# Kernel tuning notes

Hardware: AMD Instinct MI355X
Metric: run time of the kernel (lower is better)

The kernel has to match this reference:

```python
import jax, jax.numpy as jnp
import numpy as np

D_MODEL = 256
D_EDGE = 64
EPS = 1e-05
INPUT_FEATS = 2 * D_MODEL + D_EDGE + 1  # 577


def _linear_params(key, fan_in, fan_out):
    k1, k2 = jax.random.split(key)
    lim = 1.0 / np.sqrt(fan_in)
    W = jax.random.uniform(k1, (fan_in, fan_out), minval=-lim, maxval=lim, dtype=jnp.float32)
    b = jax.random.uniform(k2, (fan_out,), minval=-lim, maxval=lim, dtype=jnp.float32)
    return W, b


def setup_inputs() -> dict:
    key = jax.random.key(0)
    ks = jax.random.split(key, 16)
    B, N = 8, 128
    inp = {
        "coords": jax.random.normal(ks[0], (B, N, 3), dtype=jnp.float32),
        "inv_feats": jax.random.normal(ks[1], (B, N, D_MODEL), dtype=jnp.float32),
        "adj_matrix": jnp.ones((B, N, N), dtype=jnp.float32),
        "atom_mask": jnp.ones((B, N), dtype=jnp.float32),
        "edge_feats": jax.random.normal(ks[2], (B, N, N, D_EDGE), dtype=jnp.float32),
    }
    inp["W_e1"], inp["b_e1"] = _linear_params(ks[3], INPUT_FEATS, D_MODEL)
    inp["W_e2"], inp["b_e2"] = _linear_params(ks[4], D_MODEL, D_MODEL)
    inp["W_att"], inp["b_att"] = _linear_params(ks[5], D_MODEL, 1)
    inp["W_h1"], inp["b_h1"] = _linear_params(ks[6], 2 * D_MODEL, D_MODEL)
    inp["W_h2"], inp["b_h2"] = _linear_params(ks[7], D_MODEL, D_MODEL)
    inp["W_x1"], inp["b_x1"] = _linear_params(ks[8], INPUT_FEATS, D_MODEL)
    inp["W_x2"], inp["b_x2"] = _linear_params(ks[9], D_MODEL, D_MODEL)
    inp["W_x3"], inp["b_x3"] = _linear_params(ks[10], D_MODEL, 1)
    return inp


def _pair_linear(W, b, node_feats, ef):
    # Linear over concat([node_i, node_j, ef]) without materializing the concat.
    # W: [2*d_model + d_edge + 1, out]
    d = D_MODEL
    hi = node_feats @ W[:d]          # [B,N,out]
    hj = node_feats @ W[d:2 * d]     # [B,N,out]
    he = ef @ W[2 * d:]              # [B,N,N,out]
    return hi[:, :, None, :] + hj[:, None, :, :] + he + b


def _egnn_forward(coords, inv_feats, adj_matrix, atom_mask, edge_feats,
                  W_e1, b_e1, W_e2, b_e2, W_att, b_att,
                  W_h1, b_h1, W_h2, b_h2, W_x1, b_x1, W_x2, b_x2, W_x3, b_x3):
    mask = atom_mask[..., None]                       # [B,N,1]
    diff = coords[:, :, None, :] - coords[:, None, :, :]   # [B,N,N,3]
    sq = jnp.sum(diff * diff, axis=-1, keepdims=True)      # [B,N,N,1]
    ef = jnp.concatenate([edge_feats, sq], axis=-1)        # [B,N,N,d_edge+1]
    adj = adj_matrix[..., None]                             # [B,N,N,1]

    # phi_e: Linear-SiLU-Linear-SiLU on pair features
    msg = jax.nn.silu(_pair_linear(W_e1, b_e1, inv_feats, ef))
    msg = jax.nn.silu(msg @ W_e2 + b_e2)                    # [B,N,N,d]

    att = jax.nn.sigmoid(msg @ W_att + b_att)               # [B,N,N,1]
    node_msg = jnp.sum(msg * att * adj, axis=2)             # [B,N,d]

    h = jnp.concatenate([inv_feats, node_msg], axis=-1)
    h = jax.nn.silu(h @ W_h1 + b_h1) @ W_h2 + b_h2          # [B,N,d]

    # phi_x: Linear-SiLU-Linear-SiLU-Linear -> scalar per edge
    ex = jax.nn.silu(_pair_linear(W_x1, b_x1, inv_feats, ef))
    ex = jax.nn.silu(ex @ W_x2 + b_x2)
    edge_attn = ex @ W_x3 + b_x3                             # [B,N,N,1]

    normalisers = jnp.sqrt(sq[..., 0] + EPS) + 1.0           # [B,N,N]
    weighted = diff * edge_attn / normalisers[..., None] * adj
    coord_updates = jnp.sum(weighted, axis=2)                # [B,N,3]
    num_nodes = jnp.sum(mask, axis=1) + 1.0                  # [B,1]
    coord_updates = coord_updates / num_nodes[:, :, None]

    out_coords = (coords + coord_updates) * mask
    out_feats = h * mask
    return out_coords, out_feats


def reference(coords, inv_feats, adj_matrix, atom_mask, edge_feats,
              W_e1, b_e1, W_e2, b_e2, W_att, b_att,
              W_h1, b_h1, W_h2, b_h2, W_x1, b_x1, W_x2, b_x2, W_x3, b_x3):
    return _egnn_forward(coords, inv_feats, adj_matrix, atom_mask, edge_feats,
                         W_e1, b_e1, W_e2, b_e2, W_att, b_att,
                         W_h1, b_h1, W_h2, b_h2, W_x1, b_x1, W_x2, b_x2, W_x3, b_x3)
```

## Files before the change

kernel.cpp:

```cpp
#include <hip/hip_runtime.h>

typedef __attribute__((ext_vector_type(8))) __bf16 bf16x8;
typedef __attribute__((ext_vector_type(4))) __bf16 bf16x4;
typedef __attribute__((ext_vector_type(4))) float f32x4;

#define SCHED0 __builtin_amdgcn_sched_barrier(0)

__device__ __forceinline__ float fast_sig(float x) {
  return __builtin_amdgcn_rcpf(1.0f + __expf(-x));
}
__device__ __forceinline__ float siluf(float x) { return x * fast_sig(x); }
__device__ __forceinline__ __bf16 tobf(float x) { return (__bf16)x; }

__device__ __forceinline__ void stage16(const void* g, void* l) {
  __builtin_amdgcn_global_load_lds(
      (const __attribute__((address_space(1))) void*)g,
      (__attribute__((address_space(3))) void*)l, 16, 0, 0);
}

__device__ __forceinline__ void stage_slice(
    const __bf16* __restrict__ src, int ld, int off,
    __bf16* swbuf, int tid)
{
  const int w = tid >> 6;
  #pragma unroll
  for (int q = 0; q < 2; q++) {
    int t16 = q * 512 + tid;
    int c = t16 >> 2, slot = t16 & 3;
    int kpart = slot ^ ((c >> 1) & 3);
    const __bf16* g = src + (size_t)c * ld + off + kpart * 8;
    __bf16* l = swbuf + (size_t)(q * 512 + w * 64) * 8;
    stage16(g, l);
  }
}

__device__ __forceinline__ void stage_k(
    const __bf16* __restrict__ wt, const __bf16* __restrict__ w2,
    int k, __bf16* buf, int tid)
{
  if (k < 2) stage_slice(wt, 576, 512 + k * 32, buf, tid);
  else       stage_slice(w2, 256, (k - 2) * 32, buf, tid);
}

__global__ __launch_bounds__(256) void k_prep(
    const float* __restrict__ We1, const float* __restrict__ Wx1,
    const float* __restrict__ We2, const float* __restrict__ Wx2,
    const float* __restrict__ Wh1, const float* __restrict__ Wh2,
    const float* __restrict__ invf,
    __bf16* __restrict__ wt_e, __bf16* __restrict__ wt_x,
    __bf16* __restrict__ w2e, __bf16* __restrict__ w2x,
    __bf16* __restrict__ wh1t, __bf16* __restrict__ wh2t,
    __bf16* __restrict__ invb,
    float* __restrict__ nmsg, float* __restrict__ cupd)
{
  int idx = blockIdx.x * 256 + threadIdx.x;
  if (idx < 147456) {
    int kk = idx / 576, f = idx - kk * 576;
    wt_e[idx] = tobf(We1[f * 256 + kk]);
    wt_x[idx] = tobf(Wx1[f * 256 + kk]);
  }
  if (idx < 65536) {
    int c = idx >> 8, k = idx & 255;
    w2e[idx] = tobf(We2[k * 256 + c]);
    w2x[idx] = tobf(Wx2[k * 256 + c]);
    wh2t[idx] = tobf(Wh2[k * 256 + c]);
    f32x4 z = {0.f, 0.f, 0.f, 0.f};
    *(f32x4*)(nmsg + idx * 4) = z;
  }
  if (idx < 131072) {
    int c = idx >> 9, k = idx & 511;
    wh1t[idx] = tobf(Wh1[k * 256 + c]);
  }
  if (idx < 3072) cupd[idx] = 0.f;
  invb[idx] = tobf(invf[idx]);
}

template<int NKS>
__device__ __forceinline__ void node_gemm64(
    const __bf16* __restrict__ B, int ldb, int boff,
    const __bf16* __restrict__ A, int lda, int aoff,
    int row0, int tid, f32x4 acc[4][4])
{
  const int lane = tid & 63, wc = tid >> 6, lr = lane & 15, lg = lane >> 4;
  #pragma unroll
  for (int ks = 0; ks < NKS; ks++) {
    bf16x8 bB[4], aA[4];
    #pragma unroll
    for (int m = 0; m < 4; m++)
      bB[m] = *(const bf16x8*)(B + (size_t)(row0 + m * 16 + lr) * ldb + boff + ks * 32 + lg * 8);
    #pragma unroll
    for (int n = 0; n < 4; n++)
      aA[n] = *(const bf16x8*)(A + (size_t)(wc * 64 + n * 16 + lr) * lda + aoff + ks * 32 + lg * 8);
    #pragma unroll
    for (int m = 0; m < 4; m++)
      #pragma unroll
      for (int n = 0; n < 4; n++)
        acc[m][n] = __builtin_amdgcn_mfma_f32_16x16x32_bf16(aA[n], bB[m], acc[m][n], 0, 0, 0);
  }
}

__global__ __launch_bounds__(256) void k_nproj(
    const __bf16* __restrict__ invb,
    const __bf16* __restrict__ wt_e, const __bf16* __restrict__ wt_x,
    const float* __restrict__ be1, const float* __restrict__ bx1,
    float* __restrict__ hie, float* __restrict__ hix,
    __bf16* __restrict__ hje, __bf16* __restrict__ hjx)
{
  const int tid = threadIdx.x;
  const int row0 = blockIdx.x * 64;
  const int mat = blockIdx.y;
  const __bf16* A = (mat < 2) ? wt_e : wt_x;
  const int aoff = (mat & 1) ? 256 : 0;

  f32x4 acc[4][4];
  #pragma unroll
  for (int m = 0; m < 4; m++)
    #pragma unroll
    for (int n = 0; n < 4; n++) { f32x4 z = {0.f,0.f,0.f,0.f}; acc[m][n] = z; }
  node_gemm64<8>(invb, 256, 0, A, 576, aoff, row0, tid, acc);

  const int lane = tid & 63, wc = tid >> 6, lr = lane & 15, lg = lane >> 4;
  if ((mat & 1) == 0) {
    const float* bias = (mat == 0) ? be1 : bx1;
    float* out = (mat == 0) ? hie : hix;
    #pragma unroll
    for (int m = 0; m < 4; m++) {
      int node = row0 + m * 16 + lr;
      #pragma unroll
      for (int n = 0; n < 4; n++) {
        int c0 = wc * 64 + n * 16 + lg * 4;
        f32x4 v = acc[m][n] + *(const f32x4*)(bias + c0);
        *(f32x4*)(out + (size_t)node * 256 + c0) = v;
      }
    }
  } else {
    __bf16* out = (mat == 1) ? hje : hjx;
    #pragma unroll
    for (int m = 0; m < 4; m++) {
      int node = row0 + m * 16 + lr;
      #pragma unroll
      for (int n = 0; n < 4; n++) {
        int c0 = wc * 64 + n * 16 + lg * 4;
        bf16x4 pk;
        #pragma unroll
        for (int r = 0; r < 4; r++) pk[r] = tobf(acc[m][n][r]);
        *(bf16x4*)(out + (size_t)node * 256 + c0) = pk;
      }
    }
  }
}

__global__ __launch_bounds__(256) void k_h1(
    const __bf16* __restrict__ invb, const float* __restrict__ nmsg,
    const __bf16* __restrict__ wh1t,
    const float* __restrict__ bh1, __bf16* __restrict__ h1b)
{
  const int tid = threadIdx.x;
  const int row0 = blockIdx.x * 64;
  const int c0 = blockIdx.y * 64;
  const int lane = tid & 63, w = tid >> 6, lr = lane & 15, lg = lane >> 4;
  const int node = row0 + w * 16 + lr;

  f32x4 acc[4];
  #pragma unroll
  for (int n = 0; n < 4; n++) { f32x4 z = {0.f,0.f,0.f,0.f}; acc[n] = z; }

  #pragma unroll
  for (int ks = 0; ks < 16; ks++) {
    bf16x8 bB;
    if (ks < 8) {
      bB = *(const bf16x8*)(invb + (size_t)node * 256 + ks * 32 + lg * 8);
    } else {
      const float* pp = nmsg + (size_t)node * 256 + (ks - 8) * 32 + lg * 8;
      f32x4 lo = *(const f32x4*)pp;
      f32x4 hi = *(const f32x4*)(pp + 4);
      bf16x8 t;
      t[0]=tobf(lo[0]); t[1]=tobf(lo[1]); t[2]=tobf(lo[2]); t[3]=tobf(lo[3]);
      t[4]=tobf(hi[0]); t[5]=tobf(hi[1]); t[6]=tobf(hi[2]); t[7]=tobf(hi[3]);
      bB = t;
    }
    #pragma unroll
    for (int n = 0; n < 4; n++) {
      bf16x8 aA = *(const bf16x8*)(wh1t + (size_t)(c0 + n * 16 + lr) * 512 + ks * 32 + lg * 8);
      acc[n] = __builtin_amdgcn_mfma_f32_16x16x32_bf16(aA, bB, acc[n], 0, 0, 0);
    }
  }

  #pragma unroll
  for (int n = 0; n < 4; n++) {
    int cc = c0 + n * 16 + lg * 4;
    f32x4 b4 = *(const f32x4*)(bh1 + cc);
    bf16x4 pk;
    #pragma unroll
    for (int r = 0; r < 4; r++) pk[r] = tobf(siluf(acc[n][r] + b4[r]));
    *(bf16x4*)(h1b + (size_t)node * 256 + cc) = pk;
  }
}

__global__ __launch_bounds__(256) void k_h2(
    const __bf16* __restrict__ h1b, const __bf16* __restrict__ wh2t,
    const float* __restrict__ bh2, const float* __restrict__ amask,
    const float* __restrict__ coords, const float* __restrict__ cupd,
    float* __restrict__ out_feats, float* __restrict__ out_coords)
{
  __shared__ float sM[2];
  const int tid = threadIdx.x;
  const int row0 = blockIdx.x * 64;
  const int c0 = blockIdx.y * 64;
  const int b = row0 >> 7;
  const int lane = tid & 63, w = tid >> 6, lr = lane & 15, lg = lane >> 4;
  const int node = row0 + w * 16 + lr;

  f32x4 acc[4];
  #pragma unroll
  for (int n = 0; n < 4; n++) { f32x4 z = {0.f,0.f,0.f,0.f}; acc[n] = z; }

  #pragma unroll
  for (int ks = 0; ks < 8; ks++) {
    bf16x8 bB = *(const bf16x8*)(h1b + (size_t)node * 256 + ks * 32 + lg * 8);
    #pragma unroll
    for (int n = 0; n < 4; n++) {
      bf16x8 aA = *(const bf16x8*)(wh2t + (size_t)(c0 + n * 16 + lr) * 256 + ks * 32 + lg * 8);
      acc[n] = __builtin_amdgcn_mfma_f32_16x16x32_bf16(aA, bB, acc[n], 0, 0, 0);
    }
  }

  float msk = amask[node];
  #pragma unroll
  for (int n = 0; n < 4; n++) {
    int cc = c0 + n * 16 + lg * 4;
    f32x4 b4 = *(const f32x4*)(bh2 + cc);
    f32x4 v = (acc[n] + b4) * msk;
    *(f32x4*)(out_feats + (size_t)node * 256 + cc) = v;
  }

  if (blockIdx.y == 0) {
    if (tid < 128) {
      float v = amask[b * 128 + tid];
      #pragma unroll
      for (int off = 1; off < 64; off <<= 1) v += __shfl_xor(v, off);
      if ((tid & 63) == 0) sM[tid >> 6] = v;
    }
    __syncthreads();
    const float sNum = sM[0] + sM[1];
    if (tid < 192) {
      int nl = tid / 3, d = tid - nl * 3;
      int nd = row0 + nl;
      float upd = cupd[nd * 3 + d] / (sNum + 1.0f);
      out_coords[nd * 3 + d] = (coords[nd * 3 + d] + upd) * amask[nd];
    }
  }
}

__global__ __launch_bounds__(512, 4) void k_edge(
    const float* __restrict__ coords, const float* __restrict__ adjm,
    const float* __restrict__ ef,
    const float* __restrict__ We1, const float* __restrict__ Wx1,
    const float* __restrict__ batt,
    const float* __restrict__ be2, const float* __restrict__ bx2,
    const float* __restrict__ bx3,
    const float* __restrict__ Watt, const float* __restrict__ Wx3,
    const float* __restrict__ hie, const float* __restrict__ hix,
    const __bf16* __restrict__ hje, const __bf16* __restrict__ hjx,
    const __bf16* __restrict__ wt_e, const __bf16* __restrict__ wt_x,
    const __bf16* __restrict__ w2e, const __bf16* __restrict__ w2x,
    float* __restrict__ nmsg, float* __restrict__ cupd)
{
  __shared__ __align__(16) char sSb[64 * 512];
  __shared__ __align__(16) __bf16 sW0[8192];
  __shared__ __align__(16) __bf16 sW1[8192];
  __shared__ __align__(16) __bf16 sE[64 * 72];
  __shared__ float slaste[256], slastx[256];
  __shared__ float sqv[64], sAdj[64], sRedE[64], sRedX[64], sNM[256], sCup[4];

  const int tid = threadIdx.x;
  const int raw = blockIdx.x;
  const int lb = (raw & 7) * 256 + (raw >> 3);
  const int bi = lb >> 1;
  const int half = lb & 1;
  const int b = bi >> 7;
  const int j0g = half * 64;
  const int jg0 = b * 128 + j0g;

  const int lane = tid & 63, w = tid >> 6;
  const int lr = lane & 15, lg = lane >> 4;
  const int cg = (w & 3) * 64;
  const int jw = (w >> 2) * 32;
  const int slot = lg ^ ((lr >> 1) & 3);
  const int awbase = (cg + lr) * 32 + slot * 8;

  const float cix = coords[bi * 3 + 0];
  const float ciy = coords[bi * 3 + 1];
  const float ciz = coords[bi * 3 + 2];
  const float b0e = batt[0];
  const float b0x = bx3[0];

  if (tid < 64) { sRedE[tid] = 0.f; sRedX[tid] = 0.f; }
  else if (tid < 320) sNM[tid - 64] = 0.f;
  else if (tid < 324) sCup[tid - 320] = 0.f;
  if (tid < 256) {
    slaste[tid] = We1[576 * 256 + tid];
    slastx[tid] = Wx1[576 * 256 + tid];
  }
  if (tid >= 448) {
    int j = tid - 448;
    int jg = jg0 + j;
    float dx = cix - coords[jg * 3 + 0];
    float dy = ciy - coords[jg * 3 + 1];
    float dz = ciz - coords[jg * 3 + 2];
    sqv[j] = dx * dx + dy * dy + dz * dz;
  }
  if (tid >= 384 && tid < 448)
    sAdj[tid - 384] = adjm[(size_t)bi * 128 + j0g + (tid - 384)];

  {
    const float* efb = ef + ((size_t)bi * 128 + j0g) * 64;
    int row = tid >> 3;
    int col = (tid & 7) * 8;
    const float* er = efb + row * 64 + col;
    f32x4 x = *(const f32x4*)er;
    f32x4 y = *(const f32x4*)(er + 4);
    bf16x8 t;
    t[0] = tobf(x[0]); t[1] = tobf(x[1]); t[2] = tobf(x[2]); t[3] = tobf(x[3]);
    t[4] = tobf(y[0]); t[5] = tobf(y[1]); t[6] = tobf(y[2]); t[7] = tobf(y[3]);
    *(bf16x8*)(sE + row * 72 + col) = t;
  }

  stage_k(wt_e, w2e, 0, sW0, tid);
  stage_k(wt_e, w2e, 1, sW1, tid);

  asm volatile("s_waitcnt lgkmcnt(0)" ::: "memory");
  SCHED0;

  #pragma unroll
  for (int p = 0; p < 2; p++) {
    const __bf16* wt = p ? wt_x : wt_e;
    const __bf16* w2 = p ? w2x : w2e;
    const float* hi_g = (p ? hix : hie) + (size_t)bi * 256;
    const __bf16* hj_g = (p ? hjx : hje) + (size_t)jg0 * 256;
    const float* slast = p ? slastx : slaste;
    const float* bias2 = p ? bx2 : be2;
    const float* vvec = p ? Wx3 : Watt;
    float* sRed = p ? sRedX : sRedE;
    const float batt0 = p ? b0x : b0e;

    f32x4 acc[2][4];
    #pragma unroll
    for (int m = 0; m < 2; m++)
      #pragma unroll
      for (int n = 0; n < 4; n++) { f32x4 z = {0.f,0.f,0.f,0.f}; acc[m][n] = z; }

    #pragma unroll
    for (int k = 0; k < 10; k++) {
      SCHED0;
      if (k < 9) asm volatile("s_waitcnt vmcnt(2)" ::: "memory");
      else       asm volatile("s_waitcnt vmcnt(0)" ::: "memory");
      SCHED0;
      __builtin_amdgcn_s_barrier();
      SCHED0;

      __bf16* sw = (k & 1) ? sW1 : sW0;
      bf16x8 aW[4];
      #pragma unroll
      for (int n = 0; n < 4; n++) aW[n] = *(const bf16x8*)(sw + awbase + n * 512);

      if (k < 2) {
        bf16x8 bEf[2];
        #pragma unroll
        for (int m = 0; m < 2; m++)
          bEf[m] = *(const bf16x8*)(sE + (jw + m * 16 + lr) * 72 + k * 32 + lg * 8);
        __builtin_amdgcn_s_setprio(1);
        #pragma unroll
        for (int m = 0; m < 2; m++)
          #pragma unroll
          for (int n = 0; n < 4; n++)
            acc[m][n] = __builtin_amdgcn_mfma_f32_16x16x32_bf16(aW[n], bEf[m], acc[m][n], 0, 0, 0);
        __builtin_amdgcn_s_setprio(0);
        if (k == 1) {
          f32x4 hi4[4];
          bf16x4 hj4[2][4];
          #pragma unroll
          for (int n = 0; n < 4; n++)
            hi4[n] = *(const f32x4*)(hi_g + cg + n * 16 + lg * 4);
          #pragma unroll
          for (int m = 0; m < 2; m++) {
            const int jl = jw + m * 16 + lr;
            #pragma unroll
            for (int n = 0; n < 4; n++)
              hj4[m][n] = *(const bf16x4*)(hj_g + (size_t)jl * 256 + cg + n * 16 + lg * 4);
          }
          #pragma unroll
          for (int m = 0; m < 2; m++) {
            const int jl = jw + m * 16 + lr;
            const float sq = sqv[jl];
            #pragma unroll
            for (int n = 0; n < 4; n++) {
              const int kk0 = cg + n * 16 + lg * 4;
              f32x4 sl4 = *(const f32x4*)(slast + kk0);
              bf16x4 pk;
              #pragma unroll
              for (int r = 0; r < 4; r++) {
                float v = acc[m][n][r] + hi4[n][r] + (float)hj4[m][n][r] + sq * sl4[r];
                pk[r] = tobf(siluf(v));
              }
              int off = (jl * 512 + kk0 * 2) ^ ((jl & 7) << 4);
              *(bf16x4*)(sSb + off) = pk;
              f32x4 z = {0.f, 0.f, 0.f, 0.f};
              acc[m][n] = z;
            }
          }
        }
      } else {
        const int ks = k - 2;
        bf16x8 bS[2];
        #pragma unroll
        for (int m = 0; m < 2; m++) {
          const int jl = jw + m * 16 + lr;
          int off = (jl * 512 + (ks * 32 + lg * 8) * 2) ^ ((jl & 7) << 4);
          bS[m] = *(const bf16x8*)(sSb + off);
        }
        __builtin_amdgcn_s_setprio(1);
        #pragma unroll
        for (int m = 0; m < 2; m++)
          #pragma unroll
          for (int n = 0; n < 4; n++)
            acc[m][n] = __builtin_amdgcn_mfma_f32_16x16x32_bf16(aW[n], bS[m], acc[m][n], 0, 0, 0);
        __builtin_amdgcn_s_setprio(0);
      }

      SCHED0;
      asm volatile("s_waitcnt lgkmcnt(0)" ::: "memory");
      SCHED0;
      __builtin_amdgcn_s_barrier();
      SCHED0;
      if (k < 8) stage_k(wt, w2, k + 2, sw, tid);
    }

    if (p == 0) {
      stage_k(wt_x, w2x, 0, sW0, tid);
      stage_k(wt_x, w2x, 1, sW1, tid);
    }

    float pr[2] = {0.f, 0.f};
    #pragma unroll
    for (int n = 0; n < 4; n++) {
      f32x4 bb = *(const f32x4*)(bias2 + cg + n * 16 + lg * 4);
      f32x4 vv = *(const f32x4*)(vvec  + cg + n * 16 + lg * 4);
      #pragma unroll
      for (int m = 0; m < 2; m++)
        #pragma unroll
        for (int r = 0; r < 4; r++) {
          float s = siluf(acc[m][n][r] + bb[r]);
          acc[m][n][r] = s;
          pr[m] += s * vv[r];
        }
    }
    #pragma unroll
    for (int m = 0; m < 2; m++) {
      pr[m] += __shfl_xor(pr[m], 16);
      pr[m] += __shfl_xor(pr[m], 32);
    }
    if (lane < 16) {
      #pragma unroll
      for (int m = 0; m < 2; m++)
        atomicAdd(&sRed[jw + m * 16 + lr], pr[m]);
    }
    SCHED0;
    asm volatile("s_waitcnt lgkmcnt(0)" ::: "memory");
    SCHED0;
    __builtin_amdgcn_s_barrier();
    SCHED0;

    if (p == 0) {
      float aw[2];
      #pragma unroll
      for (int m = 0; m < 2; m++) {
        int jl = jw + m * 16 + lr;
        aw[m] = fast_sig(sRed[jl] + batt0) * sAdj[jl];
      }
      f32x4 q[4];
      #pragma unroll
      for (int n = 0; n < 4; n++) { f32x4 z = {0.f,0.f,0.f,0.f}; q[n] = z; }
      #pragma unroll
      for (int m = 0; m < 2; m++)
        #pragma unroll
        for (int n = 0; n < 4; n++)
          q[n] += acc[m][n] * aw[m];
      #pragma unroll
      for (int off = 1; off < 16; off <<= 1)
        #pragma unroll
        for (int n = 0; n < 4; n++)
          #pragma unroll
          for (int r = 0; r < 4; r++)
            q[n][r] += __shfl_xor(q[n][r], off);
      if (lr == 0) {
        #pragma unroll
        for (int n = 0; n < 4; n++)
          #pragma unroll
          for (int r = 0; r < 4; r++)
            atomicAdd(&sNM[cg + n * 16 + lg * 4 + r], q[n][r]);
      }
    } else {
      if (tid < 64) {
        int jl = tid;
        int jgl = jg0 + jl;
        float ea = sRed[jl] + batt0;
        float wgt = ea * __builtin_amdgcn_rcpf(sqrtf(sqv[jl] + 1e-5f) + 1.0f) * sAdj[jl];
        float wx = wgt * (cix - coords[jgl * 3 + 0]);
        float wy = wgt * (ciy - coords[jgl * 3 + 1]);
        float wz = wgt * (ciz - coords[jgl * 3 + 2]);
        #pragma unroll
        for (int off = 1; off < 64; off <<= 1) {
          wx += __shfl_xor(wx, off);
          wy += __shfl_xor(wy, off);
          wz += __shfl_xor(wz, off);
        }
        if (tid == 0) { sCup[0] = wx; sCup[1] = wy; sCup[2] = wz; }
      }
    }
  }

  __syncthreads();
  if (tid < 256) atomicAdd(&nmsg[(size_t)bi * 256 + tid], sNM[tid]);
  if (tid < 3) atomicAdd(&cupd[bi * 3 + tid], sCup[tid]);
}

extern "C" void kernel_launch(void* const* d_in, const int* in_sizes, int n_in,
                              void* d_out, int out_size, void* d_ws, size_t ws_size,
                              hipStream_t stream)
{
  const float* coords = (const float*)d_in[0];
  const float* invf  = (const float*)d_in[1];
  const float* adjm  = (const float*)d_in[2];
  const float* amask = (const float*)d_in[3];
  const float* ef    = (const float*)d_in[4];
  const float* We1   = (const float*)d_in[5];
  const float* be1   = (const float*)d_in[6];
  const float* We2   = (const float*)d_in[7];
  const float* be2   = (const float*)d_in[8];
  const float* Watt  = (const float*)d_in[9];
  const float* batt  = (const float*)d_in[10];
  const float* Wh1   = (const float*)d_in[11];
  const float* bh1   = (const float*)d_in[12];
  const float* Wh2   = (const float*)d_in[13];
  const float* bh2   = (const float*)d_in[14];
  const float* Wx1   = (const float*)d_in[15];
  const float* bx1   = (const float*)d_in[16];
  const float* Wx2   = (const float*)d_in[17];
  const float* bx2   = (const float*)d_in[18];
  const float* Wx3   = (const float*)d_in[19];
  const float* bx3   = (const float*)d_in[20];

  char* ws = (char*)d_ws;
  const size_t MB = 1u << 20;
  float*  hie  = (float*)(ws + 0 * MB);
  float*  hix  = (float*)(ws + 1 * MB);
  __bf16* hje  = (__bf16*)(ws + 2 * MB);
  __bf16* hjx  = (__bf16*)(ws + 2 * MB + 524288);
  __bf16* invb = (__bf16*)(ws + 3 * MB);
  __bf16* h1b  = (__bf16*)(ws + 3 * MB + 524288);
  size_t woff = 4 * MB;
  __bf16* wt_e = (__bf16*)(ws + woff);
  __bf16* wt_x = (__bf16*)(ws + woff + 294912);
  __bf16* w2e  = (__bf16*)(ws + woff + 2 * 294912);
  __bf16* w2x  = (__bf16*)(ws + woff + 2 * 294912 + 131072);
  __bf16* wh1t = (__bf16*)(ws + woff + 2 * 294912 + 2 * 131072);
  __bf16* wh2t = (__bf16*)(ws + woff + 2 * 294912 + 2 * 131072 + 262144);
  float*  nmsg = (float*)(ws + 5 * MB + 524288);
  float*  cupd = (float*)(ws + 6 * MB + 524288);

  float* out_coords = (float*)d_out;
  float* out_feats  = out_coords + 8 * 128 * 3;

  hipLaunchKernelGGL(k_prep, dim3(1024), dim3(256), 0, stream,
                     We1, Wx1, We2, Wx2, Wh1, Wh2, invf,
                     wt_e, wt_x, w2e, w2x, wh1t, wh2t, invb, nmsg, cupd);
  hipLaunchKernelGGL(k_nproj, dim3(16, 4), dim3(256), 0, stream,
                     invb, wt_e, wt_x, be1, bx1, hie, hix, hje, hjx);
  hipLaunchKernelGGL(k_edge, dim3(2048), dim3(512), 0, stream,
                     coords, adjm, ef, We1, Wx1, batt, be2, bx2, bx3, Watt, Wx3,
                     hie, hix, hje, hjx, wt_e, wt_x, w2e, w2x, nmsg, cupd);
  hipLaunchKernelGGL(k_h1, dim3(16, 4), dim3(256), 0, stream,
                     invb, nmsg, wh1t, bh1, h1b);
  hipLaunchKernelGGL(k_h2, dim3(16, 4), dim3(256), 0, stream,
                     h1b, wh2t, bh2, amask, coords, cupd, out_feats, out_coords);
}
```

Measured before the change: 154.6 us.

## Give each wave private weight slices to drop per-step block barriers

Changes the warp work split in the edge kernel. Each of the 8 waves now owns 32 output channels and all 64 edges, instead of a 64-channel by 32-edge tile. Each wave stages its own weight slice into a per-wave LDS region, so the block-wide barrier around every K step can be removed. Only one barrier remains, after the first-layer activation write, because the shared activations still need to be synchronised. The next pass's weight prefetch is also folded into the tail of the loop. In exchange, B-operand LDS reads per wave double, and each wave now waits on its own global-to-LDS loads without cross-wave sharing.

```diff
diff --git a/kernel.cpp b/kernel.cpp
--- a/kernel.cpp
+++ b/kernel.cpp
@@ -18,28 +18,23 @@
       (__attribute__((address_space(3))) void*)l, 16, 0, 0);
 }
 
-__device__ __forceinline__ void stage_slice(
+__device__ __forceinline__ void stage_pw(
     const __bf16* __restrict__ src, int ld, int off,
-    __bf16* swbuf, int tid)
-{
-  const int w = tid >> 6;
+    __bf16* dst, int lane, int cg)
+{
   #pragma unroll
   for (int q = 0; q < 2; q++) {
-    int t16 = q * 512 + tid;
-    int c = t16 >> 2, slot = t16 & 3;
-    int kpart = slot ^ ((c >> 1) & 3);
-    const __bf16* g = src + (size_t)c * ld + off + kpart * 8;
-    __bf16* l = swbuf + (size_t)(q * 512 + w * 64) * 8;
-    stage16(g, l);
-  }
-}
-
-__device__ __forceinline__ void stage_k(
+    const __bf16* g = src + (size_t)(cg + q * 16 + (lane & 15)) * ld + off + (lane >> 4) * 8;
+    stage16(g, dst + q * 512);
+  }
+}
+
+__device__ __forceinline__ void stage_pw_k(
     const __bf16* __restrict__ wt, const __bf16* __restrict__ w2,
-    int k, __bf16* buf, int tid)
-{
-  if (k < 2) stage_slice(wt, 576, 512 + k * 32, buf, tid);
-  else       stage_slice(w2, 256, (k - 2) * 32, buf, tid);
+    int k, __bf16* dst, int lane, int cg)
+{
+  if (k < 2) stage_pw(wt, 576, 512 + k * 32, dst, lane, cg);
+  else       stage_pw(w2, 256, (k - 2) * 32, dst, lane, cg);
 }
 
 __global__ __launch_bounds__(256) void k_prep(
@@ -267,8 +262,7 @@
     float* __restrict__ nmsg, float* __restrict__ cupd)
 {
   __shared__ __align__(16) char sSb[64 * 512];
-  __shared__ __align__(16) __bf16 sW0[8192];
-  __shared__ __align__(16) __bf16 sW1[8192];
+  __shared__ __align__(16) __bf16 sW[2][8][1024];
   __shared__ __align__(16) __bf16 sE[64 * 72];
   __shared__ float slaste[256], slastx[256];
   __shared__ float sqv[64], sAdj[64], sRedE[64], sRedX[64], sNM[256], sCup[4];
@@ -282,18 +276,19 @@
   const int j0g = half * 64;
   const int jg0 = b * 128 + j0g;
 
-  const int lane = tid & 63, w = tid >> 6;
+  const int lane = tid & 63;
+  const int wv = tid >> 6;
   const int lr = lane & 15, lg = lane >> 4;
-  const int cg = (w & 3) * 64;
-  const int jw = (w >> 2) * 32;
-  const int slot = lg ^ ((lr >> 1) & 3);
-  const int awbase = (cg + lr) * 32 + slot * 8;
+  const int cg = wv * 32;
 
   const float cix = coords[bi * 3 + 0];
   const float ciy = coords[bi * 3 + 1];
   const float ciz = coords[bi * 3 + 2];
   const float b0e = batt[0];
   const float b0x = bx3[0];
+
+  stage_pw(wt_e, 576, 512, &sW[0][wv][0], lane, cg);
+  stage_pw(wt_e, 576, 544, &sW[1][wv][0], lane, cg);
 
   if (tid < 64) { sRedE[tid] = 0.f; sRedX[tid] = 0.f; }
   else if (tid < 320) sNM[tid - 64] = 0.f;
@@ -326,10 +321,9 @@
     *(bf16x8*)(sE + row * 72 + col) = t;
   }
 
-  stage_k(wt_e, w2e, 0, sW0, tid);
-  stage_k(wt_e, w2e, 1, sW1, tid);
-
+  SCHED0;
   asm volatile("s_waitcnt lgkmcnt(0)" ::: "memory");
+  __builtin_amdgcn_s_barrier();
   SCHED0;
 
   #pragma unroll
@@ -344,110 +338,102 @@
     float* sRed = p ? sRedX : sRedE;
     const float batt0 = p ? b0x : b0e;
 
-    f32x4 acc[2][4];
-    #pragma unroll
-    for (int m = 0; m < 2; m++)
-      #pragma unroll
-      for (int n = 0; n < 4; n++) { f32x4 z = {0.f,0.f,0.f,0.f}; acc[m][n] = z; }
+    f32x4 acc[4][2];
+    #pragma unroll
+    for (int m = 0; m < 4; m++)
+      #pragma unroll
+      for (int n = 0; n < 2; n++) { f32x4 z = {0.f,0.f,0.f,0.f}; acc[m][n] = z; }
 
     #pragma unroll
     for (int k = 0; k < 10; k++) {
       SCHED0;
-      if (k < 9) asm volatile("s_waitcnt vmcnt(2)" ::: "memory");
-      else       asm volatile("s_waitcnt vmcnt(0)" ::: "memory");
+      if (p == 1 && k == 9) asm volatile("s_waitcnt vmcnt(0)" ::: "memory");
+      else                  asm volatile("s_waitcnt vmcnt(2)" ::: "memory");
       SCHED0;
-      __builtin_amdgcn_s_barrier();
-      SCHED0;
-
-      __bf16* sw = (k & 1) ? sW1 : sW0;
-      bf16x8 aW[4];
-      #pragma unroll
-      for (int n = 0; n < 4; n++) aW[n] = *(const bf16x8*)(sw + awbase + n * 512);
-
+
+      const __bf16* swp = &sW[k & 1][wv][0];
+      bf16x8 aW[2];
+      #pragma unroll
+      for (int n = 0; n < 2; n++)
+        aW[n] = *(const bf16x8*)(swp + n * 512 + lg * 128 + lr * 8);
+
+      bf16x8 bX[4];
       if (k < 2) {
-        bf16x8 bEf[2];
-        #pragma unroll
-        for (int m = 0; m < 2; m++)
-          bEf[m] = *(const bf16x8*)(sE + (jw + m * 16 + lr) * 72 + k * 32 + lg * 8);
-        __builtin_amdgcn_s_setprio(1);
-        #pragma unroll
-        for (int m = 0; m < 2; m++)
+        #pragma unroll
+        for (int m = 0; m < 4; m++)
+          bX[m] = *(const bf16x8*)(sE + (m * 16 + lr) * 72 + k * 32 + lg * 8);
+      } else {
+        const int ks = k - 2;
+        #pragma unroll
+        for (int m = 0; m < 4; m++) {
+          const int jl = m * 16 + lr;
+          int off = (jl * 512 + (ks * 32 + lg * 8) * 2) ^ ((jl & 7) << 4);
+          bX[m] = *(const bf16x8*)(sSb + off);
+        }
+      }
+
+      __builtin_amdgcn_s_setprio(1);
+      #pragma unroll
+      for (int m = 0; m < 4; m++)
+        #pragma unroll
+        for (int n = 0; n < 2; n++)
+          acc[m][n] = __builtin_amdgcn_mfma_f32_16x16x32_bf16(aW[n], bX[m], acc[m][n], 0, 0, 0);
+      __builtin_amdgcn_s_setprio(0);
+
+      if (k == 1) {
+        f32x4 hi4[2];
+        bf16x4 hj4[4][2];
+        #pragma unroll
+        for (int n = 0; n < 2; n++)
+          hi4[n] = *(const f32x4*)(hi_g + cg + n * 16 + lg * 4);
+        #pragma unroll
+        for (int m = 0; m < 4; m++) {
+          const int jl = m * 16 + lr;
           #pragma unroll
-          for (int n = 0; n < 4; n++)
-            acc[m][n] = __builtin_amdgcn_mfma_f32_16x16x32_bf16(aW[n], bEf[m], acc[m][n], 0, 0, 0);
-        __builtin_amdgcn_s_setprio(0);
-        if (k == 1) {
-          f32x4 hi4[4];
-          bf16x4 hj4[2][4];
+          for (int n = 0; n < 2; n++)
+            hj4[m][n] = *(const bf16x4*)(hj_g + (size_t)jl * 256 + cg + n * 16 + lg * 4);
+        }
+        #pragma unroll
+        for (int m = 0; m < 4; m++) {
+          const int jl = m * 16 + lr;
+          const float sq = sqv[jl];
           #pragma unroll
-          for (int n = 0; n < 4; n++)
-            hi4[n] = *(const f32x4*)(hi_g + cg + n * 16 + lg * 4);
-          #pragma unroll
-          for (int m = 0; m < 2; m++) {
-            const int jl = jw + m * 16 + lr;
+          for (int n = 0; n < 2; n++) {
+            const int kk0 = cg + n * 16 + lg * 4;
+            f32x4 sl4 = *(const f32x4*)(slast + kk0);
+            bf16x4 pk;
             #pragma unroll
-            for (int n = 0; n < 4; n++)
-              hj4[m][n] = *(const bf16x4*)(hj_g + (size_t)jl * 256 + cg + n * 16 + lg * 4);
-          }
-          #pragma unroll
-          for (int m = 0; m < 2; m++) {
-            const int jl = jw + m * 16 + lr;
-            const float sq = sqv[jl];
-            #pragma unroll
-            for (int n = 0; n < 4; n++) {
-              const int kk0 = cg + n * 16 + lg * 4;
-              f32x4 sl4 = *(const f32x4*)(slast + kk0);
-              bf16x4 pk;
-              #pragma unroll
-              for (int r = 0; r < 4; r++) {
-                float v = acc[m][n][r] + hi4[n][r] + (float)hj4[m][n][r] + sq * sl4[r];
-                pk[r] = tobf(siluf(v));
-              }
-              int off = (jl * 512 + kk0 * 2) ^ ((jl & 7) << 4);
-              *(bf16x4*)(sSb + off) = pk;
-              f32x4 z = {0.f, 0.f, 0.f, 0.f};
-              acc[m][n] = z;
+            for (int r = 0; r < 4; r++) {
+              float v = acc[m][n][r] + hi4[n][r] + (float)hj4[m][n][r] + sq * sl4[r];
+              pk[r] = tobf(siluf(v));
             }
+            int off = (jl * 512 + kk0 * 2) ^ ((jl & 7) << 4);
+            *(bf16x4*)(sSb + off) = pk;
+            f32x4 z = {0.f, 0.f, 0.f, 0.f};
+            acc[m][n] = z;
           }
         }
-      } else {
-        const int ks = k - 2;
-        bf16x8 bS[2];
-        #pragma unroll
-        for (int m = 0; m < 2; m++) {
-          const int jl = jw + m * 16 + lr;
-          int off = (jl * 512 + (ks * 32 + lg * 8) * 2) ^ ((jl & 7) << 4);
-          bS[m] = *(const bf16x8*)(sSb + off);
-        }
-        __builtin_amdgcn_s_setprio(1);
-        #pragma unroll
-        for (int m = 0; m < 2; m++)
-          #pragma unroll
-          for (int n = 0; n < 4; n++)
-            acc[m][n] = __builtin_amdgcn_mfma_f32_16x16x32_bf16(aW[n], bS[m], acc[m][n], 0, 0, 0);
-        __builtin_amdgcn_s_setprio(0);
+        SCHED0;
+        asm volatile("s_waitcnt lgkmcnt(0)" ::: "memory");
+        __builtin_amdgcn_s_barrier();
+        SCHED0;
       }
 
       SCHED0;
       asm volatile("s_waitcnt lgkmcnt(0)" ::: "memory");
       SCHED0;
-      __builtin_amdgcn_s_barrier();
-      SCHED0;
-      if (k < 8) stage_k(wt, w2, k + 2, sw, tid);
-    }
-
-    if (p == 0) {
-      stage_k(wt_x, w2x, 0, sW0, tid);
-      stage_k(wt_x, w2x, 1, sW1, tid);
-    }
-
-    float pr[2] = {0.f, 0.f};
-    #pragma unroll
-    for (int n = 0; n < 4; n++) {
+      __bf16* dst = &sW[k & 1][wv][0];
+      if (k < 8)       stage_pw_k(wt, w2, k + 2, dst, lane, cg);
+      else if (p == 0) stage_pw_k(wt_x, w2x, k - 8, dst, lane, cg);
+    }
+
+    float pr[4] = {0.f, 0.f, 0.f, 0.f};
+    #pragma unroll
+    for (int n = 0; n < 2; n++) {
       f32x4 bb = *(const f32x4*)(bias2 + cg + n * 16 + lg * 4);
       f32x4 vv = *(const f32x4*)(vvec  + cg + n * 16 + lg * 4);
       #pragma unroll
-      for (int m = 0; m < 2; m++)
+      for (int m = 0; m < 4; m++)
         #pragma unroll
         for (int r = 0; r < 4; r++) {
           float s = siluf(acc[m][n][r] + bb[r]);
@@ -456,46 +442,43 @@
         }
     }
     #pragma unroll
-    for (int m = 0; m < 2; m++) {
+    for (int m = 0; m < 4; m++) {
       pr[m] += __shfl_xor(pr[m], 16);
       pr[m] += __shfl_xor(pr[m], 32);
     }
     if (lane < 16) {
       #pragma unroll
-      for (int m = 0; m < 2; m++)
-        atomicAdd(&sRed[jw + m * 16 + lr], pr[m]);
+      for (int m = 0; m < 4; m++)
+        atomicAdd(&sRed[m * 16 + lr], pr[m]);
     }
     SCHED0;
     asm volatile("s_waitcnt lgkmcnt(0)" ::: "memory");
-    SCHED0;
     __builtin_amdgcn_s_barrier();
     SCHED0;
 
     if (p == 0) {
-      float aw[2];
-      #pragma unroll
-      for (int m = 0; m < 2; m++) {
-        int jl = jw + m * 16 + lr;
-        aw[m] = fast_sig(sRed[jl] + batt0) * sAdj[jl];
-      }
-      f32x4 q[4];
-      #pragma unroll
-      for (int n = 0; n < 4; n++) { f32x4 z = {0.f,0.f,0.f,0.f}; q[n] = z; }
-      #pragma unroll
-      for (int m = 0; m < 2; m++)
-        #pragma unroll
-        for (int n = 0; n < 4; n++)
+      float aw[4];
+      #pragma unroll
+      for (int m = 0; m < 4; m++)
+        aw[m] = fast_sig(sRed[m * 16 + lr] + batt0) * sAdj[m * 16 + lr];
+      f32x4 q[2];
+      #pragma unroll
+      for (int n = 0; n < 2; n++) { f32x4 z = {0.f,0.f,0.f,0.f}; q[n] = z; }
+      #pragma unroll
+      for (int m = 0; m < 4; m++)
+        #pragma unroll
+        for (int n = 0; n < 2; n++)
           q[n] += acc[m][n] * aw[m];
       #pragma unroll
       for (int off = 1; off < 16; off <<= 1)
         #pragma unroll
-        for (int n = 0; n < 4; n++)
+        for (int n = 0; n < 2; n++)
           #pragma unroll
           for (int r = 0; r < 4; r++)
             q[n][r] += __shfl_xor(q[n][r], off);
       if (lr == 0) {
         #pragma unroll
-        for (int n = 0; n < 4; n++)
+        for (int n = 0; n < 2; n++)
           #pragma unroll
           for (int r = 0; r < 4; r++)
             atomicAdd(&sNM[cg + n * 16 + lg * 4 + r], q[n][r]);
```

After: 185.9 us. 1.2x slower.
